# Kernel optimization log

Measured on AMD Instinct MI355X. Metric: run time of the kernel, lower is better.

Reference implementation:

```python
import jax, jax.numpy as jnp
import numpy as np

NL, H, PD, NH, NB = 4, 256, 64, 4, 65
B, L, AA = 2, 384, 48
DH = H // NH
MAX_REL = 32


def _ln(x, g, b):
    m = x.mean(-1, keepdims=True)
    v = ((x - m) ** 2).mean(-1, keepdims=True)
    return (x - m) * jax.lax.rsqrt(v + 1e-5) * g + b


def setup_inputs() -> dict:
    key = jax.random.key(0)
    ks = iter(jax.random.split(key, 64))
    w = lambda *s: jax.random.normal(next(ks), s, jnp.float32) * 0.02
    return dict(
        x=jax.random.normal(next(ks), (B, L, AA), jnp.float32),
        rp_w=w(AA, H), rp_b=jnp.zeros((H,), jnp.float32),
        pos_embed=w(L, H),
        pii_w=w(H, PD), pii_b=jnp.zeros((PD,), jnp.float32),
        pij_w=w(H, PD), pij_b=jnp.zeros((PD,), jnp.float32),
        rel_emb=w(2 * MAX_REL + 2, PD),
        ln_seq_g=jnp.ones((NL, H), jnp.float32), ln_seq_b=jnp.zeros((NL, H), jnp.float32),
        ln_pair_g=jnp.ones((NL, PD), jnp.float32), ln_pair_b=jnp.zeros((NL, PD), jnp.float32),
        pb_w=w(NL, PD, NH),
        in_w=w(NL, H, 3 * H), in_b=jnp.zeros((NL, 3 * H), jnp.float32),
        out_w=w(NL, H, H), out_b=jnp.zeros((NL, H), jnp.float32),
        ff_ln_g=jnp.ones((NL, H), jnp.float32), ff_ln_b=jnp.zeros((NL, H), jnp.float32),
        ff_w1=w(NL, H, 4 * H), ff_b1=jnp.zeros((NL, 4 * H), jnp.float32),
        ff_w2=w(NL, 4 * H, H), ff_b2=jnp.zeros((NL, H), jnp.float32),
        pu_ln_g=jnp.ones((NL, PD), jnp.float32), pu_ln_b=jnp.zeros((NL, PD), jnp.float32),
        pu_w1=w(NL, PD, PD), pu_b1=jnp.zeros((NL, PD), jnp.float32),
        pu_w2=w(NL, PD, PD), pu_b2=jnp.zeros((NL, PD), jnp.float32),
        outer_w=w(NL, 2 * H, PD), outer_b=jnp.zeros((NL, PD), jnp.float32),
        dh_ln_g=jnp.ones((PD,), jnp.float32), dh_ln_b=jnp.zeros((PD,), jnp.float32),
        dh_w1=w(PD, PD), dh_b1=jnp.zeros((PD,), jnp.float32),
        dh_w2=w(PD, NB), dh_b2=jnp.zeros((NB,), jnp.float32),
    )


def reference(x, rp_w, rp_b, pos_embed, pii_w, pii_b, pij_w, pij_b, rel_emb,
              ln_seq_g, ln_seq_b, ln_pair_g, ln_pair_b, pb_w, in_w, in_b,
              out_w, out_b, ff_ln_g, ff_ln_b, ff_w1, ff_b1, ff_w2, ff_b2,
              pu_ln_g, pu_ln_b, pu_w1, pu_b1, pu_w2, pu_b2, outer_w, outer_b,
              dh_ln_g, dh_ln_b, dh_w1, dh_b1, dh_w2, dh_b2):
    Bx, Lx, _ = x.shape
    gelu = lambda t: jax.nn.gelu(t, approximate=False)  # torch nn.GELU default (erf)
    h = x @ rp_w + rp_b + pos_embed[:Lx][None]
    # pair init: outer sum of two linear projections + clipped rel-pos embedding
    pair = (h @ pii_w + pii_b)[:, :, None, :] + (h @ pij_w + pij_b)[:, None, :, :]
    idx = jnp.arange(Lx)
    rel = jnp.clip(idx[None, :] - idx[:, None], -MAX_REL, MAX_REL) + MAX_REL  # (L,L)
    pair = pair + rel_emb[rel][None]
    for i in range(NL):
        seq_n = _ln(h, ln_seq_g[i], ln_seq_b[i])
        bias = _ln(pair, ln_pair_g[i], ln_pair_b[i]) @ pb_w[i]  # (B,L,L,NH)
        mask = bias.mean(axis=(0, 3))  # torch: permute->reshape(B*NH,L,L)->mean(0)
        qkv = seq_n @ in_w[i] + in_b[i]
        q, k, v = jnp.split(qkv, 3, axis=-1)
        q = q.reshape(Bx, Lx, NH, DH)
        k = k.reshape(Bx, Lx, NH, DH)
        v = v.reshape(Bx, Lx, NH, DH)
        scores = jnp.einsum('blhd,bmhd->bhlm', q, k) / float(np.sqrt(DH)) + mask
        attn = jax.nn.softmax(scores, axis=-1)
        o = jnp.einsum('bhlm,bmhd->blhd', attn, v).reshape(Bx, Lx, H)
        h = h + o @ out_w[i] + out_b[i]
        h = h + gelu(_ln(h, ff_ln_g[i], ff_ln_b[i]) @ ff_w1[i] + ff_b1[i]) @ ff_w2[i] + ff_b2[i]
        # outer_proj(cat([h_i, h_j])) == h@W[:H] outer-summed with h@W[H:]
        oi = h @ outer_w[i][:H]
        oj = h @ outer_w[i][H:]
        outer = oi[:, :, None, :] + oj[:, None, :, :] + outer_b[i]  # (B,L,L,PD)
        pair = pair + gelu(_ln(outer, pu_ln_g[i], pu_ln_b[i]) @ pu_w1[i] + pu_b1[i]) @ pu_w2[i] + pu_b2[i]
    logits = gelu(_ln(pair, dh_ln_g, dh_ln_b) @ dh_w1 + dh_b1) @ dh_w2 + dh_b2
    return (logits + jnp.swapaxes(logits, 1, 2)) / 2.0
```

## Files before the change

### kernel.cpp

```cpp
#include <hip/hip_runtime.h>
#include <math.h>

#define LSEQ 384
#define HD 256
#define PDIM 64
#define NHEAD 4
#define NBINS 65
#define BATCH 2
#define NTT (LSEQ / 16)
#define NTRI (NTT * (NTT + 1) / 2)

typedef __attribute__((ext_vector_type(8))) short bf16x8;
typedef __attribute__((ext_vector_type(16))) float f32x16;
typedef __attribute__((ext_vector_type(4))) float f32x4;
typedef __attribute__((ext_vector_type(4))) unsigned u32x4;
typedef __attribute__((ext_vector_type(4))) short s16x4;
#define MFMA32(a, b, c) __builtin_amdgcn_mfma_f32_32x32x16_bf16(a, b, c, 0, 0, 0)

template<int CTRL, int RMASK>
__device__ __forceinline__ float dpp_sum_step(float v) {
    int x = __builtin_amdgcn_update_dpp(0, __float_as_int(v), CTRL, RMASK, 0xf, true);
    return v + __int_as_float(x);
}
template<int CTRL, int RMASK>
__device__ __forceinline__ float dpp_max_step(float v) {
    int x = __builtin_amdgcn_update_dpp(__float_as_int(v), __float_as_int(v), CTRL, RMASK, 0xf, false);
    return fmaxf(v, __int_as_float(x));
}
__device__ __forceinline__ float wsum(float v) {
    v = dpp_sum_step<0x111, 0xf>(v);
    v = dpp_sum_step<0x112, 0xf>(v);
    v = dpp_sum_step<0x114, 0xf>(v);
    v = dpp_sum_step<0x118, 0xf>(v);
    v = dpp_sum_step<0x142, 0xa>(v);
    v = dpp_sum_step<0x143, 0xc>(v);
    return __int_as_float(__builtin_amdgcn_readlane(__float_as_int(v), 63));
}
__device__ __forceinline__ float wmax(float v) {
    v = dpp_max_step<0x111, 0xf>(v);
    v = dpp_max_step<0x112, 0xf>(v);
    v = dpp_max_step<0x114, 0xf>(v);
    v = dpp_max_step<0x118, 0xf>(v);
    v = dpp_max_step<0x142, 0xa>(v);
    v = dpp_max_step<0x143, 0xc>(v);
    return __int_as_float(__builtin_amdgcn_readlane(__float_as_int(v), 63));
}
__device__ __forceinline__ float gelu_erf(float x) {
    return 0.5f * x * (1.0f + erff(x * 0.70710678f));
}

__device__ __forceinline__ unsigned short f2bf(float x) {
    unsigned u = __float_as_uint(x);
    unsigned r = (u + 0x7fff + ((u >> 16) & 1)) >> 16;
    return (unsigned short)r;
}
__device__ __forceinline__ float bf2f(unsigned short h) {
    return __uint_as_float(((unsigned)h) << 16);
}
__device__ __forceinline__ void split_bf(float x, unsigned short& h, unsigned short& l) {
    h = f2bf(x);
    l = f2bf(x - bf2f(h));
}

__device__ __forceinline__ unsigned cvt_pk_bf(float lo, float hi) {
    unsigned r;
    asm("v_cvt_pk_bf16_f32 %0, %1, %2" : "=v"(r) : "v"(lo), "v"(hi));
    return r;
}
__device__ __forceinline__ void pack8(const float* v, u32x4& h, u32x4& l) {
#pragma unroll
    for (int j = 0; j < 4; ++j) {
        float a = v[2 * j], b = v[2 * j + 1];
        unsigned hp = cvt_pk_bf(a, b);
        float ra = a - __uint_as_float(hp << 16);
        float rb = b - __uint_as_float(hp & 0xffff0000u);
        h[j] = hp;
        l[j] = cvt_pk_bf(ra, rb);
    }
}
__device__ __forceinline__ bf16x8 as_bf(u32x4 x) {
    union { u32x4 u; bf16x8 b; } c; c.u = x; return c.b;
}
__device__ __forceinline__ bf16x8 ld8(const short* p) {
    s16x4 a = *(const s16x4*)p;
    s16x4 b = *(const s16x4*)(p + 4);
    bf16x8 r;
    r[0] = a[0]; r[1] = a[1]; r[2] = a[2]; r[3] = a[3];
    r[4] = b[0]; r[5] = b[1]; r[6] = b[2]; r[7] = b[3];
    return r;
}

__global__ void k_h_init(const float* __restrict__ x, const float* __restrict__ rp_w,
                         const float* __restrict__ rp_b, const float* __restrict__ pos,
                         float* __restrict__ h) {
    __shared__ float xs[48];
    int row = blockIdx.x;
    int l = row % LSEQ;
    int t = threadIdx.x;
    if (t < 48) xs[t] = x[row * 48 + t];
    __syncthreads();
    float acc = rp_b[t] + pos[l * HD + t];
#pragma unroll 8
    for (int a = 0; a < 48; ++a) acc += xs[a] * rp_w[a * HD + t];
    h[row * HD + t] = acc;
}

__global__ void k_proj2(const float* __restrict__ h, const float* __restrict__ wA,
                        const float* __restrict__ wB, const float* __restrict__ bA,
                        const float* __restrict__ bB, int center,
                        float* __restrict__ pA, float* __restrict__ pB) {
    __shared__ float hs[HD];
    int row = blockIdx.x;
    int t = threadIdx.x;
    hs[t] = h[row * HD + t];
    hs[t + 128] = h[row * HD + t + 128];
    __syncthreads();
    int col = t & 63;
    const float* w = (t < 64) ? wA : wB;
    const float* bias = (t < 64) ? bA : bB;
    float acc = bias ? bias[col] : 0.0f;
#pragma unroll 8
    for (int a = 0; a < HD; ++a) acc += hs[a] * w[a * PDIM + col];
    if (center) {
        float mean = wsum(acc) * (1.0f / PDIM);
        acc -= mean;
    }
    float* p = (t < 64) ? pA : pB;
    p[row * PDIM + col] = acc;
}

__global__ void __launch_bounds__(64) k_pair_init2(
    const float* __restrict__ pi, const float* __restrict__ pj,
    const float* __restrict__ rel_emb, const float* __restrict__ gpb,
    const float* __restrict__ cbv, float* __restrict__ pair,
    float* __restrict__ mask_out) {
    __shared__ __align__(16) float pt[32][65];
    int blk = blockIdx.x;
    int row = blk / 12, seg = blk % 12;
    int b = row / LSEQ, i = row % LSEQ;
    int t = threadIdx.x;
    int pl = t & 31, hq = t >> 5;
    int j0 = seg * 32;
    float piv = pi[row * 64 + t];
    const float* pjb = pj + ((size_t)b * LSEQ + j0) * 64;
#pragma unroll 8
    for (int j = 0; j < 32; ++j) {
        int r = j0 + j - i; r = r < -32 ? -32 : (r > 32 ? 32 : r); r += 32;
        pt[j][t] = piv + pjb[j * 64 + t] + rel_emb[r * 64 + t];
    }
    __syncthreads();
    float4* dst4 = (float4*)(pair + ((size_t)row * LSEQ + j0) * 64);
    for (int n = t; n < 512; n += 64) {
        int r2 = n >> 4, c4 = (n & 15) << 2;
        float4 g4 = { pt[r2][c4], pt[r2][c4 + 1], pt[r2][c4 + 2], pt[r2][c4 + 3] };
        dst4[n] = g4;
    }
    float vv[32];
    float sv = 0.0f;
#pragma unroll
    for (int c = 0; c < 32; ++c) { vv[c] = pt[pl][hq * 32 + c]; sv += vv[c]; }
    sv += __shfl_xor(sv, 32);
    float mean = sv * (1.0f / PDIM);
    float sd2 = 0.0f, sdg = 0.0f;
#pragma unroll
    for (int c = 0; c < 32; ++c) {
        float d = vv[c] - mean;
        sd2 = fmaf(d, d, sd2);
        sdg = fmaf(d, gpb[hq * 32 + c], sdg);
    }
    sd2 += __shfl_xor(sd2, 32);
    sdg += __shfl_xor(sdg, 32);
    float rsv = rsqrtf(sd2 * (1.0f / PDIM) + 1e-5f);
    float dot = rsv * sdg + cbv[0];
    if (hq == 0)
        atomicAdd(mask_out + i * LSEQ + j0 + pl, dot * (1.0f / (BATCH * NHEAD)));
}

__global__ void k_prep(const float* __restrict__ pu_ln_g, const float* __restrict__ pu_ln_b,
                       const float* __restrict__ pu_w1, const float* __restrict__ pu_b1,
                       const float* __restrict__ pu_w2,
                       const float* __restrict__ dh_ln_g, const float* __restrict__ dh_ln_b,
                       const float* __restrict__ dh_w1, const float* __restrict__ dh_b1,
                       const float* __restrict__ dh_w2,
                       unsigned short* __restrict__ w1hT, unsigned short* __restrict__ w1lT,
                       unsigned short* __restrict__ w2hT, unsigned short* __restrict__ w2lT,
                       float* __restrict__ b1p, float* __restrict__ w2c) {
    int i = blockIdx.x;
    int c = threadIdx.x;
    const float *g, *bb, *w1, *b1, *w2;
    int w2s;
    if (i < 4) { g = pu_ln_g + i * 64; bb = pu_ln_b + i * 64; w1 = pu_w1 + i * 4096;
                 b1 = pu_b1 + i * 64; w2 = pu_w2 + i * 4096; w2s = 64; }
    else       { g = dh_ln_g; bb = dh_ln_b; w1 = dh_w1; b1 = dh_b1; w2 = dh_w2; w2s = 65; }
    float accb = b1[c];
    for (int k = 0; k < 64; ++k) {
        float wv = w1[k * 64 + c];
        accb += bb[k] * wv;
        unsigned short h, l;
        split_bf(g[k] * wv, h, l);
        w1hT[i * 4096 + c * 64 + k] = h;
        w1lT[i * 4096 + c * 64 + k] = l;
        split_bf(w2[k * w2s + c], h, l);
        w2hT[i * 4096 + c * 64 + k] = h;
        w2lT[i * 4096 + c * 64 + k] = l;
    }
    b1p[i * 64 + c] = accb;
    if (i == 4) w2c[c] = dh_w2[c * 65 + 64];
}

__global__ void k_maskprep(const float* __restrict__ g, const float* __restrict__ bb,
                           const float* __restrict__ pbw, float* __restrict__ gp,
                           float* __restrict__ cb) {
    int li = blockIdx.x;
    int c = threadIdx.x;
    const float* pw = pbw + li * PDIM * NHEAD;
    float pbs = pw[c * 4] + pw[c * 4 + 1] + pw[c * 4 + 2] + pw[c * 4 + 3];
    gp[li * 64 + c] = g[li * 64 + c] * pbs;
    float s = wsum(bb[li * 64 + c] * pbs);
    if (c == 0) cb[li] = s;
}

__global__ void k_split_T(const float* __restrict__ src, unsigned short* __restrict__ dh,
                          unsigned short* __restrict__ dl, int K, int N,
                          int tiles_k, int tiles_n, size_t sstride, size_t dstride) {
    __shared__ float lds[64][65];
    int bid = blockIdx.x;
    int tpl = tiles_k * tiles_n;
    int layer = bid / tpl;
    int rest = bid % tpl;
    int kt = rest / tiles_n, nt = rest % tiles_n;
    const float* s = src + layer * sstride;
    int t = threadIdx.x, c = t & 63, r0 = t >> 6;
    for (int r = r0; r < 64; r += 4)
        lds[r][c] = s[(size_t)(kt * 64 + r) * N + nt * 64 + c];
    __syncthreads();
    unsigned short* oh = dh + layer * dstride;
    unsigned short* ol = dl + layer * dstride;
    for (int r = r0; r < 64; r += 4) {
        float v = lds[c][r];
        unsigned short h, l;
        split_bf(v, h, l);
        size_t o = (size_t)(nt * 64 + r) * K + kt * 64 + c;
        oh[o] = h;
        ol[o] = l;
    }
}

template<bool GELU>
__global__ void __launch_bounds__(256) k_gemm(
    const float* __restrict__ X, const unsigned short* __restrict__ wTh,
    const unsigned short* __restrict__ wTl, const float* __restrict__ bias,
    const float* __restrict__ R, float* __restrict__ OUT, int K, int N) {
    int idx = blockIdx.x * 4 + (threadIdx.x >> 6);
    int lane = threadIdx.x & 63;
    int pl = lane & 31, hq = lane >> 5;
    int ntiles = N >> 5;
    int mt = idx / ntiles, nt = idx % ntiles;
    const float* xr = X + (size_t)(mt * 32 + pl) * K + 8 * hq;
    const unsigned short* bh = wTh + (size_t)(nt * 32 + pl) * K + 8 * hq;
    const unsigned short* bl = wTl + (size_t)(nt * 32 + pl) * K + 8 * hq;
    int n = nt * 32 + pl;
    float bv = bias[n];
    f32x16 acc;
#pragma unroll
    for (int r = 0; r < 16; ++r) {
        int mr = mt * 32 + (r & 3) + 8 * (r >> 2) + 4 * hq;
        acc[r] = bv + (R ? R[(size_t)mr * N + n] : 0.0f);
    }
#pragma unroll 4
    for (int s = 0; s < K; s += 16) {
        const f32x4* x4 = (const f32x4*)(xr + s);
        f32x4 xa = x4[0], xb = x4[1];
        float xv[8];
#pragma unroll
        for (int j = 0; j < 4; ++j) { xv[j] = xa[j]; xv[4 + j] = xb[j]; }
        u32x4 ah, al;
        pack8(xv, ah, al);
        bf16x8 bhv = *(const bf16x8*)(bh + s);
        bf16x8 blv = *(const bf16x8*)(bl + s);
        acc = MFMA32(as_bf(ah), bhv, acc);
        acc = MFMA32(as_bf(al), bhv, acc);
        acc = MFMA32(as_bf(ah), blv, acc);
    }
#pragma unroll
    for (int r = 0; r < 16; ++r) {
        int mr = mt * 32 + (r & 3) + 8 * (r >> 2) + 4 * hq;
        float v = acc[r];
        OUT[(size_t)mr * N + n] = GELU ? gelu_erf(v) : v;
    }
}

__global__ void k_ln_seq(const float* __restrict__ h, const float* __restrict__ g,
                         const float* __restrict__ b, float* __restrict__ out) {
    __shared__ float red[8];
    int row = blockIdx.x;
    int t = threadIdx.x;
    int w = t >> 6, lane = t & 63;
    float v = h[row * HD + t];
    float s = wsum(v);
    if (lane == 0) red[w] = s;
    __syncthreads();
    float mean = (red[0] + red[1] + red[2] + red[3]) * (1.0f / HD);
    float d = v - mean;
    float q = wsum(d * d);
    if (lane == 0) red[4 + w] = q;
    __syncthreads();
    float var = (red[4] + red[5] + red[6] + red[7]) * (1.0f / HD);
    out[row * HD + t] = d * rsqrtf(var + 1e-5f) * g[t] + b[t];
}

__global__ void k_attn(const float* __restrict__ qkv, const float* __restrict__ mask,
                       float* __restrict__ o) {
    __shared__ __align__(16) float qs[64];
    __shared__ float sc[LSEQ];
    __shared__ float red[8];
    __shared__ float op[4][64];
    int bid = blockIdx.x;
    int l = bid % LSEQ;
    int nh = (bid / LSEQ) & 3;
    int b = bid / (LSEQ * NHEAD);
    int t = threadIdx.x;
    int w = t >> 6, lane = t & 63;
    const float* qbase = qkv + ((size_t)(b * LSEQ + l)) * 768 + nh * 64;
    if (t < 64) qs[t] = qbase[t];
    __syncthreads();
    float lmax = -1e30f;
    float myv[2];
#pragma unroll
    for (int it = 0; it < 2; ++it) {
        int m = t + it * 256;
        if (m < LSEQ) {
            const float* kb = qkv + ((size_t)(b * LSEQ + m)) * 768 + 256 + nh * 64;
            const float4* k4 = (const float4*)kb;
            const float4* q4 = (const float4*)qs;
            float acc = 0.0f;
#pragma unroll
            for (int a = 0; a < 16; ++a) {
                float4 kv = k4[a], qv = q4[a];
                acc += qv.x * kv.x + qv.y * kv.y + qv.z * kv.z + qv.w * kv.w;
            }
            float s = acc * 0.125f + mask[l * LSEQ + m];
            myv[it] = s;
            lmax = fmaxf(lmax, s);
        } else myv[it] = -1e30f;
    }
    float wm = wmax(lmax);
    if (lane == 0) red[w] = wm;
    __syncthreads();
    float gmax = fmaxf(fmaxf(red[0], red[1]), fmaxf(red[2], red[3]));
    float lsum = 0.0f;
#pragma unroll
    for (int it = 0; it < 2; ++it) {
        int m = t + it * 256;
        if (m < LSEQ) {
            float e = expf(myv[it] - gmax);
            sc[m] = e;
            lsum += e;
        }
    }
    float ws = wsum(lsum);
    if (lane == 0) red[4 + w] = ws;
    __syncthreads();
    float inv = 1.0f / (red[4] + red[5] + red[6] + red[7]);
    int d = t & 63, gq = t >> 6;
    float part = 0.0f;
    for (int m = gq * 96; m < (gq + 1) * 96; ++m)
        part += sc[m] * qkv[((size_t)(b * LSEQ + m)) * 768 + 512 + nh * 64 + d];
    op[gq][d] = part;
    __syncthreads();
    if (t < 64) {
        float ov = (op[0][t] + op[1][t] + op[2][t] + op[3][t]) * inv;
        o[((size_t)(b * LSEQ + l)) * HD + nh * 64 + t] = ov;
    }
}

template<bool DIST>
__global__ void __launch_bounds__(256) k_pair_upd(
    const float* __restrict__ ojc,
    const float* __restrict__ oic,
    const unsigned short* __restrict__ w1hT, const unsigned short* __restrict__ w1lT,
    const float* __restrict__ b1p,
    const unsigned short* __restrict__ w2hT, const unsigned short* __restrict__ w2lT,
    const float* __restrict__ b2, float* __restrict__ pair,
    const float* __restrict__ gpb, const float* __restrict__ cbv,
    float* __restrict__ mask_out,
    const unsigned short* __restrict__ dw1h, const unsigned short* __restrict__ dw1l,
    const float* __restrict__ db1p,
    const unsigned short* __restrict__ dw2h, const unsigned short* __restrict__ dw2l,
    const float* __restrict__ w2c, const float* __restrict__ db2,
    float* __restrict__ outg) {
    __shared__ short lw[4][64][68];
    constexpr int PTR = DIST ? 128 : 1;
    __shared__ __align__(16) float pt[PTR][65];
    int blk = blockIdx.x;
    int row = blk / 3, seg = blk % 3;
    int b = row / LSEQ;
    int t = threadIdx.x;
    int wave = t >> 6, lane = t & 63;
    int pl = lane & 31, hq = lane >> 5;
    int jj = wave * 32 + pl;
    int p = seg * 128 + jj;
    const float* ojr = ojc + ((size_t)b * LSEQ + p) * 64;
    const float* oir = oic + (size_t)row * 64;
    float* prp = pair + ((size_t)row * LSEQ + p) * 64;

    float v[32];
    {
        const f32x4* a4 = (const f32x4*)ojr;
        const f32x4* c4 = (const f32x4*)oir;
#pragma unroll
        for (int s = 0; s < 4; ++s) {
            f32x4 a = a4[4 * s + 2 * hq], aa = a4[4 * s + 2 * hq + 1];
            f32x4 c = c4[4 * s + 2 * hq], cc = c4[4 * s + 2 * hq + 1];
#pragma unroll
            for (int j = 0; j < 4; ++j) {
                v[8 * s + j] = a[j] + c[j];
                v[8 * s + 4 + j] = aa[j] + cc[j];
            }
        }
    }
#define STAGE_W(a2, src) \
    for (int idx = t; idx < 2048; idx += 256) { \
        int rr2 = idx >> 5, cc2 = idx & 31; \
        *(unsigned*)(&lw[a2][rr2][cc2 * 2]) = *(const unsigned*)(src + rr2 * 64 + cc2 * 2); \
    }
    STAGE_W(0, w1hT)
    STAGE_W(1, w1lT)
    STAGE_W(2, w2hT)
    STAGE_W(3, w2lT)

    float ss = 0.0f;
#pragma unroll
    for (int i = 0; i < 32; ++i) ss = fmaf(v[i], v[i], ss);
    ss += __shfl_xor(ss, 32);
    float rs = rsqrtf(ss * (1.0f / PDIM) + 1e-5f);
#pragma unroll
    for (int i = 0; i < 32; ++i) v[i] *= rs;
    u32x4 zh[4], zl[4];
#pragma unroll
    for (int s = 0; s < 4; ++s) pack8(v + 8 * s, zh[s], zl[s]);

    const f32x4* b14 = (const f32x4*)b1p;
    f32x4 bi0[4], bi1[4];
#pragma unroll
    for (int g = 0; g < 4; ++g) { bi0[g] = b14[2 * g + hq]; bi1[g] = b14[8 + 2 * g + hq]; }

    __syncthreads();

    f32x16 acc0, acc1;
#pragma unroll
    for (int r = 0; r < 16; ++r) {
        acc0[r] = bi0[r >> 2][r & 3];
        acc1[r] = bi1[r >> 2][r & 3];
    }
#pragma unroll
    for (int s = 0; s < 4; ++s) {
        int ko = 16 * s + 8 * hq;
        bf16x8 a0h = ld8(&lw[0][pl][ko]);
        bf16x8 a0l = ld8(&lw[1][pl][ko]);
        bf16x8 a1h = ld8(&lw[0][32 + pl][ko]);
        bf16x8 a1l = ld8(&lw[1][32 + pl][ko]);
        bf16x8 zhs = as_bf(zh[s]), zls = as_bf(zl[s]);
        acc0 = MFMA32(a0h, zhs, acc0);
        acc0 = MFMA32(a0h, zls, acc0);
        acc0 = MFMA32(a0l, zhs, acc0);
        acc1 = MFMA32(a1h, zhs, acc1);
        acc1 = MFMA32(a1h, zls, acc1);
        acc1 = MFMA32(a1l, zhs, acc1);
    }
    float u0[16], u1[16];
#pragma unroll
    for (int r = 0; r < 16; ++r) { u0[r] = gelu_erf(acc0[r]); u1[r] = gelu_erf(acc1[r]); }

    f32x4 r0[4], r1[4], q0[4], q1[4];
    {
        const f32x4* pr4 = (const f32x4*)prp;
        const f32x4* b24 = (const f32x4*)b2;
#pragma unroll
        for (int g = 0; g < 4; ++g) {
            r0[g] = pr4[2 * g + hq];
            r1[g] = pr4[8 + 2 * g + hq];
            q0[g] = b24[2 * g + hq];
            q1[g] = b24[8 + 2 * g + hq];
        }
    }

    float rA0[4], rB0[4], rA1[4], rB1[4];
#pragma unroll
    for (int i = 0; i < 4; ++i) {
        rA0[i] = __shfl_xor(hq ? u0[i] : u0[4 + i], 32);
        rB0[i] = __shfl_xor(hq ? u0[8 + i] : u0[12 + i], 32);
        rA1[i] = __shfl_xor(hq ? u1[i] : u1[4 + i], 32);
        rB1[i] = __shfl_xor(hq ? u1[8 + i] : u1[12 + i], 32);
    }
    u32x4 uh[4], ul[4];
#pragma unroll
    for (int s = 0; s < 4; ++s) {
        int tt = s >> 1, q = s & 1;
        float fg[8];
#pragma unroll
        for (int i = 0; i < 4; ++i) {
            float own_f = q ? (tt ? u1[8 + i] : u0[8 + i]) : (tt ? u1[i] : u0[i]);
            float own_s = q ? (tt ? u1[12 + i] : u0[12 + i]) : (tt ? u1[4 + i] : u0[4 + i]);
            float rcv   = q ? (tt ? rB1[i] : rB0[i]) : (tt ? rA1[i] : rA0[i]);
            fg[i]     = hq ? rcv : own_f;
            fg[4 + i] = hq ? own_s : rcv;
        }
        pack8(fg, uh[s], ul[s]);
    }

    f32x16 c0, c1;
#pragma unroll
    for (int r = 0; r < 16; ++r) {
        int g = r >> 2, i = r & 3;
        c0[r] = q0[g][i] + r0[g][i];
        c1[r] = q1[g][i] + r1[g][i];
    }
#pragma unroll
    for (int s = 0; s < 4; ++s) {
        int ko = 16 * s + 8 * hq;
        bf16x8 a0h = ld8(&lw[2][pl][ko]);
        bf16x8 a0l = ld8(&lw[3][pl][ko]);
        bf16x8 a1h = ld8(&lw[2][32 + pl][ko]);
        bf16x8 a1l = ld8(&lw[3][32 + pl][ko]);
        bf16x8 uhs = as_bf(uh[s]), uls = as_bf(ul[s]);
        c0 = MFMA32(a0h, uhs, c0);
        c0 = MFMA32(a0h, uls, c0);
        c0 = MFMA32(a0l, uhs, c0);
        c1 = MFMA32(a1h, uhs, c1);
        c1 = MFMA32(a1h, uls, c1);
        c1 = MFMA32(a1l, uhs, c1);
    }

    if constexpr (!DIST) {
        const f32x4* gp4 = (const f32x4*)gpb;
        f32x4 gp0[4], gp1[4];
#pragma unroll
        for (int g = 0; g < 4; ++g) { gp0[g] = gp4[2 * g + hq]; gp1[g] = gp4[8 + 2 * g + hq]; }
        float sv = 0.0f;
#pragma unroll
        for (int r = 0; r < 16; ++r) sv += c0[r] + c1[r];
        sv += __shfl_xor(sv, 32);
        float mean = sv * (1.0f / PDIM);
        float sd2 = 0.0f, sdg = 0.0f;
#pragma unroll 4
        for (int r = 0; r < 16; ++r) {
            int g = r >> 2, i = r & 3;
            float d0 = c0[r] - mean, d1 = c1[r] - mean;
            sd2 = fmaf(d0, d0, sd2);
            sd2 = fmaf(d1, d1, sd2);
            sdg = fmaf(d0, gp0[g][i], sdg);
            sdg = fmaf(d1, gp1[g][i], sdg);
        }
        sd2 += __shfl_xor(sd2, 32);
        sdg += __shfl_xor(sdg, 32);
        float rsv = rsqrtf(sd2 * (1.0f / PDIM) + 1e-5f);
        float dot = rsv * sdg + cbv[0];
        if (hq == 0)
            atomicAdd(mask_out + (row % LSEQ) * LSEQ + p, dot * (1.0f / (BATCH * NHEAD)));
        f32x4* pw4 = (f32x4*)prp;
#pragma unroll
        for (int g = 0; g < 4; ++g) {
            f32x4 s0, s1;
#pragma unroll
            for (int i = 0; i < 4; ++i) { s0[i] = c0[4 * g + i]; s1[i] = c1[4 * g + i]; }
            pw4[2 * g + hq] = s0;
            pw4[8 + 2 * g + hq] = s1;
        }
    } else {
#pragma unroll
        for (int r = 0; r < 16; ++r) {
            int rr = (r & 3) + 8 * (r >> 2) + 4 * hq;
            pt[jj][rr] = c0[r];
            pt[jj][32 + rr] = c1[r];
        }
        float v2[32];
#pragma unroll
        for (int s = 0; s < 4; ++s) {
            int k0 = 16 * s + 8 * hq;
#pragma unroll
            for (int j = 0; j < 8; ++j) v2[8 * s + j] = pt[jj][k0 + j];
        }
        float sm = 0.0f;
#pragma unroll
        for (int i = 0; i < 32; ++i) sm += v2[i];
        sm += __shfl_xor(sm, 32);
        float mean = sm * (1.0f / PDIM);
        float ss2 = 0.0f;
#pragma unroll
        for (int i = 0; i < 32; ++i) { v2[i] -= mean; ss2 = fmaf(v2[i], v2[i], ss2); }
        ss2 += __shfl_xor(ss2, 32);
        float rs2 = rsqrtf(ss2 * (1.0f / PDIM) + 1e-5f);
#pragma unroll
        for (int i = 0; i < 32; ++i) v2[i] *= rs2;
#pragma unroll
        for (int s = 0; s < 4; ++s) pack8(v2 + 8 * s, zh[s], zl[s]);

        __syncthreads();
        STAGE_W(0, dw1h)
        STAGE_W(1, dw1l)
        STAGE_W(2, dw2h)
        STAGE_W(3, dw2l)
        const f32x4* d14 = (const f32x4*)db1p;
        const f32x4* d24 = (const f32x4*)db2;
        const f32x4* wc4 = (const f32x4*)w2c;
        f32x4 di0[4], di1[4], e0[4], e1[4], wc0[4], wc1[4];
#pragma unroll
        for (int g = 0; g < 4; ++g) {
            di0[g] = d14[2 * g + hq]; di1[g] = d14[8 + 2 * g + hq];
            e0[g] = d24[2 * g + hq];  e1[g] = d24[8 + 2 * g + hq];
            wc0[g] = wc4[2 * g + hq]; wc1[g] = wc4[8 + 2 * g + hq];
        }
        __syncthreads();

#pragma unroll
        for (int r = 0; r < 16; ++r) {
            acc0[r] = di0[r >> 2][r & 3];
            acc1[r] = di1[r >> 2][r & 3];
        }
#pragma unroll
        for (int s = 0; s < 4; ++s) {
            int ko = 16 * s + 8 * hq;
            bf16x8 a0h = ld8(&lw[0][pl][ko]);
            bf16x8 a0l = ld8(&lw[1][pl][ko]);
            bf16x8 a1h = ld8(&lw[0][32 + pl][ko]);
            bf16x8 a1l = ld8(&lw[1][32 + pl][ko]);
            bf16x8 zhs = as_bf(zh[s]), zls = as_bf(zl[s]);
            acc0 = MFMA32(a0h, zhs, acc0);
            acc0 = MFMA32(a0h, zls, acc0);
            acc0 = MFMA32(a0l, zhs, acc0);
            acc1 = MFMA32(a1h, zhs, acc1);
            acc1 = MFMA32(a1h, zls, acc1);
            acc1 = MFMA32(a1l, zhs, acc1);
        }
        float p64 = 0.0f;
#pragma unroll
        for (int r = 0; r < 16; ++r) {
            int g = r >> 2, i = r & 3;
            u0[r] = gelu_erf(acc0[r]);
            u1[r] = gelu_erf(acc1[r]);
            p64 = fmaf(u0[r], wc0[g][i], p64);
            p64 = fmaf(u1[r], wc1[g][i], p64);
        }
        p64 += __shfl_xor(p64, 32);
#pragma unroll
        for (int i = 0; i < 4; ++i) {
            rA0[i] = __shfl_xor(hq ? u0[i] : u0[4 + i], 32);
            rB0[i] = __shfl_xor(hq ? u0[8 + i] : u0[12 + i], 32);
            rA1[i] = __shfl_xor(hq ? u1[i] : u1[4 + i], 32);
            rB1[i] = __shfl_xor(hq ? u1[8 + i] : u1[12 + i], 32);
        }
#pragma unroll
        for (int s = 0; s < 4; ++s) {
            int tt = s >> 1, q = s & 1;
            float fg[8];
#pragma unroll
            for (int i = 0; i < 4; ++i) {
                float own_f = q ? (tt ? u1[8 + i] : u0[8 + i]) : (tt ? u1[i] : u0[i]);
                float own_s = q ? (tt ? u1[12 + i] : u0[12 + i]) : (tt ? u1[4 + i] : u0[4 + i]);
                float rcv   = q ? (tt ? rB1[i] : rB0[i]) : (tt ? rA1[i] : rA0[i]);
                fg[i]     = hq ? rcv : own_f;
                fg[4 + i] = hq ? own_s : rcv;
            }
            pack8(fg, uh[s], ul[s]);
        }
#pragma unroll
        for (int r = 0; r < 16; ++r) {
            c0[r] = e0[r >> 2][r & 3];
            c1[r] = e1[r >> 2][r & 3];
        }
#pragma unroll
        for (int s = 0; s < 4; ++s) {
            int ko = 16 * s + 8 * hq;
            bf16x8 a0h = ld8(&lw[2][pl][ko]);
            bf16x8 a0l = ld8(&lw[3][pl][ko]);
            bf16x8 a1h = ld8(&lw[2][32 + pl][ko]);
            bf16x8 a1l = ld8(&lw[3][32 + pl][ko]);
            bf16x8 uhs = as_bf(uh[s]), uls = as_bf(ul[s]);
            c0 = MFMA32(a0h, uhs, c0);
            c0 = MFMA32(a0h, uls, c0);
            c0 = MFMA32(a0l, uhs, c0);
            c1 = MFMA32(a1h, uhs, c1);
            c1 = MFMA32(a1h, uls, c1);
            c1 = MFMA32(a1l, uhs, c1);
        }
#pragma unroll
        for (int r = 0; r < 16; ++r) {
            int rr = (r & 3) + 8 * (r >> 2) + 4 * hq;
            pt[jj][rr] = c0[r];
            pt[jj][32 + rr] = c1[r];
        }
        if (hq == 0) pt[jj][64] = p64 + db2[64];
        __syncthreads();
        float4* dst = (float4*)(outg + ((size_t)row * LSEQ + seg * 128) * NBINS);
        const float4* srcl = (const float4*)&pt[0][0];
        for (int n = t; n < 128 * NBINS / 4; n += 256) dst[n] = srcl[n];
    }
#undef STAGE_W
}

__global__ void k_sym(float* __restrict__ out) {
    int u = blockIdx.x;
    int b = 0;
    if (u >= NTRI) { b = 1; u -= NTRI; }
    int lt = 0, rem = NTT;
    while (u >= rem) { u -= rem; ++lt; --rem; }
    int mt = lt + u;
    int t = threadIdx.x;
    int g = t >> 6, lane = t & 63;
    float* ob = out + (size_t)b * LSEQ * LSEQ * NBINS;
    for (int e = g; e < 256; e += 4) {
        int i = e >> 4, j = e & 15;
        if (lt == mt && j < i) continue;
        size_t ia = ((size_t)(lt * 16 + i) * LSEQ + (mt * 16 + j)) * NBINS;
        size_t ib = ((size_t)(mt * 16 + j) * LSEQ + (lt * 16 + i)) * NBINS;
        for (int k = lane; k < NBINS; k += 64) {
            float a = ob[ia + k], c = ob[ib + k];
            float vv = 0.5f * (a + c);
            ob[ia + k] = vv;
            if (ia != ib) ob[ib + k] = vv;
        }
    }
}

extern "C" void kernel_launch(void* const* d_in, const int* in_sizes, int n_in,
                              void* d_out, int out_size, void* d_ws, size_t ws_size,
                              hipStream_t stream) {
    const float* x        = (const float*)d_in[0];
    const float* rp_w     = (const float*)d_in[1];
    const float* rp_b     = (const float*)d_in[2];
    const float* pos      = (const float*)d_in[3];
    const float* pii_w    = (const float*)d_in[4];
    const float* pii_b    = (const float*)d_in[5];
    const float* pij_w    = (const float*)d_in[6];
    const float* pij_b    = (const float*)d_in[7];
    const float* rel_emb  = (const float*)d_in[8];
    const float* ln_seq_g = (const float*)d_in[9];
    const float* ln_seq_b = (const float*)d_in[10];
    const float* ln_pair_g= (const float*)d_in[11];
    const float* ln_pair_b= (const float*)d_in[12];
    const float* pb_w     = (const float*)d_in[13];
    const float* in_w     = (const float*)d_in[14];
    const float* in_b     = (const float*)d_in[15];
    const float* out_w    = (const float*)d_in[16];
    const float* out_b    = (const float*)d_in[17];
    const float* ff_ln_g  = (const float*)d_in[18];
    const float* ff_ln_b  = (const float*)d_in[19];
    const float* ff_w1    = (const float*)d_in[20];
    const float* ff_b1    = (const float*)d_in[21];
    const float* ff_w2    = (const float*)d_in[22];
    const float* ff_b2    = (const float*)d_in[23];
    const float* pu_ln_g  = (const float*)d_in[24];
    const float* pu_ln_b  = (const float*)d_in[25];
    const float* pu_w1    = (const float*)d_in[26];
    const float* pu_b1    = (const float*)d_in[27];
    const float* pu_w2    = (const float*)d_in[28];
    const float* pu_b2    = (const float*)d_in[29];
    const float* outer_w  = (const float*)d_in[30];
    const float* outer_b  = (const float*)d_in[31];
    const float* dh_ln_g  = (const float*)d_in[32];
    const float* dh_ln_b  = (const float*)d_in[33];
    const float* dh_w1    = (const float*)d_in[34];
    const float* dh_b1    = (const float*)d_in[35];
    const float* dh_w2    = (const float*)d_in[36];
    const float* dh_b2    = (const float*)d_in[37];
    float* outp = (float*)d_out;

    float* W = (float*)d_ws;
    float* h    = W;  W += BATCH * LSEQ * HD;
    float* sn   = W;  W += BATCH * LSEQ * HD;
    float* qkv  = W;  W += BATCH * LSEQ * 3 * HD;
    float* ob   = W;  W += BATCH * LSEQ * HD;
    float* mid  = W;  W += BATCH * LSEQ * 4 * HD;
    float* maskA= W;  W += LSEQ * LSEQ;
    float* maskB= W;  W += LSEQ * LSEQ;
    float* poi  = W;  W += BATCH * LSEQ * PDIM;
    float* poj  = W;  W += BATCH * LSEQ * PDIM;
    float* b1p  = W;  W += 5 * 64;
    float* w2c  = W;  W += 64;
    float* gpb  = W;  W += 4 * 64;
    float* cbv  = W;  W += 64;
    unsigned short* w1hT = (unsigned short*)W;  W += 5 * 2048;
    unsigned short* w1lT = (unsigned short*)W;  W += 5 * 2048;
    unsigned short* w2hT = (unsigned short*)W;  W += 5 * 2048;
    unsigned short* w2lT = (unsigned short*)W;  W += 5 * 2048;
    unsigned short* qwT_h = (unsigned short*)W;  W += 4 * 196608 / 2;
    unsigned short* qwT_l = (unsigned short*)W;  W += 4 * 196608 / 2;
    unsigned short* owT_h = (unsigned short*)W;  W += 4 * 65536 / 2;
    unsigned short* owT_l = (unsigned short*)W;  W += 4 * 65536 / 2;
    unsigned short* f1T_h = (unsigned short*)W;  W += 4 * 262144 / 2;
    unsigned short* f1T_l = (unsigned short*)W;  W += 4 * 262144 / 2;
    unsigned short* f2T_h = (unsigned short*)W;  W += 4 * 262144 / 2;
    unsigned short* f2T_l = (unsigned short*)W;  W += 4 * 262144 / 2;
    float* pair = W;  W += (size_t)BATCH * LSEQ * LSEQ * PDIM;

    const int rows = BATCH * LSEQ;

    k_prep<<<5, 64, 0, stream>>>(pu_ln_g, pu_ln_b, pu_w1, pu_b1, pu_w2,
                                 dh_ln_g, dh_ln_b, dh_w1, dh_b1, dh_w2,
                                 w1hT, w1lT, w2hT, w2lT, b1p, w2c);
    k_maskprep<<<4, 64, 0, stream>>>(ln_pair_g, ln_pair_b, pb_w, gpb, cbv);
    k_split_T<<<4 * 4 * 12, 256, 0, stream>>>(in_w,  qwT_h, qwT_l, 256, 768,  4, 12, 196608, 196608);
    k_split_T<<<4 * 4 * 4,  256, 0, stream>>>(out_w, owT_h, owT_l, 256, 256,  4, 4,  65536,  65536);
    k_split_T<<<4 * 4 * 16, 256, 0, stream>>>(ff_w1, f1T_h, f1T_l, 256, 1024, 4, 16, 262144, 262144);
    k_split_T<<<4 * 16 * 4, 256, 0, stream>>>(ff_w2, f2T_h, f2T_l, 1024, 256, 16, 4, 262144, 262144);
    k_h_init<<<rows, 256, 0, stream>>>(x, rp_w, rp_b, pos, h);
    k_proj2<<<rows, 128, 0, stream>>>(h, pii_w, pij_w, pii_b, pij_b, 0, poi, poj);
    hipMemsetAsync(maskA, 0, LSEQ * LSEQ * sizeof(float), stream);
    k_pair_init2<<<rows * 12, 64, 0, stream>>>(poi, poj, rel_emb, gpb, cbv, pair, maskA);

    float* mcur = maskA;
    float* mnext = maskB;
    for (int i = 0; i < 4; ++i) {
        k_ln_seq<<<rows, 256, 0, stream>>>(h, ln_seq_g + i * HD, ln_seq_b + i * HD, sn);
        k_gemm<false><<<144, 256, 0, stream>>>(sn, qwT_h + i * 196608, qwT_l + i * 196608,
                                               in_b + i * 768, nullptr, qkv, 256, 768);
        k_attn<<<BATCH * NHEAD * LSEQ, 256, 0, stream>>>(qkv, mcur, ob);
        k_gemm<false><<<48, 256, 0, stream>>>(ob, owT_h + i * 65536, owT_l + i * 65536,
                                              out_b + i * 256, h, h, 256, 256);
        k_ln_seq<<<rows, 256, 0, stream>>>(h, ff_ln_g + i * HD, ff_ln_b + i * HD, sn);
        k_gemm<true><<<192, 256, 0, stream>>>(sn, f1T_h + i * 262144, f1T_l + i * 262144,
                                              ff_b1 + i * 1024, nullptr, mid, 256, 1024);
        k_gemm<false><<<48, 256, 0, stream>>>(mid, f2T_h + i * 262144, f2T_l + i * 262144,
                                              ff_b2 + i * 256, h, h, 1024, 256);
        k_proj2<<<rows, 128, 0, stream>>>(h, outer_w + i * 2 * HD * PDIM,
                                          outer_w + i * 2 * HD * PDIM + HD * PDIM,
                                          outer_b + i * PDIM, nullptr, 1, poi, poj);
        if (i < 3) {
            hipMemsetAsync(mnext, 0, LSEQ * LSEQ * sizeof(float), stream);
            k_pair_upd<false><<<rows * 3, 256, 0, stream>>>(
                poj, poi,
                w1hT + i * 4096, w1lT + i * 4096, b1p + i * 64,
                w2hT + i * 4096, w2lT + i * 4096, pu_b2 + i * PDIM, pair,
                gpb + (i + 1) * 64, cbv + (i + 1), mnext,
                nullptr, nullptr, nullptr, nullptr, nullptr, nullptr, nullptr, nullptr);
            float* tmp = mcur; mcur = mnext; mnext = tmp;
        } else {
            k_pair_upd<true><<<rows * 3, 256, 0, stream>>>(
                poj, poi,
                w1hT + 3 * 4096, w1lT + 3 * 4096, b1p + 3 * 64,
                w2hT + 3 * 4096, w2lT + 3 * 4096, pu_b2 + 3 * PDIM, pair,
                nullptr, nullptr, nullptr,
                w1hT + 4 * 4096, w1lT + 4 * 4096, b1p + 4 * 64,
                w2hT + 4 * 4096, w2lT + 4 * 4096, w2c, dh_b2, outp);
        }
    }

    k_sym<<<2 * NTRI, 256, 0, stream>>>(outp);
}
```

Baseline: 1.117 ms.

## Halve pair-update LDS footprint, use shuffles for transpose, single-wave GEMM blocks

The pair-update kernel now stages only two weight matrices (hi/lo) in shared memory at a time, reloading the second layer's weights after a barrier. This halves static LDS usage so more blocks can be resident per CU. The distogram path replaces an LDS round-trip transpose with cross-half-wave shuffles, and the output tile aliases the same buffer. The GEMM kernel changes from four waves per block to one wave per block, with four times as many blocks. The cost is extra barriers and serialized weight staging in the pair kernel.

```diff
diff --git a/kernel.cpp b/kernel.cpp
--- a/kernel.cpp
+++ b/kernel.cpp
@@ -247,11 +247,11 @@
 }
 
 template<bool GELU>
-__global__ void __launch_bounds__(256) k_gemm(
+__global__ void __launch_bounds__(64) k_gemm(
     const float* __restrict__ X, const unsigned short* __restrict__ wTh,
     const unsigned short* __restrict__ wTl, const float* __restrict__ bias,
     const float* __restrict__ R, float* __restrict__ OUT, int K, int N) {
-    int idx = blockIdx.x * 4 + (threadIdx.x >> 6);
+    int idx = blockIdx.x;
     int lane = threadIdx.x & 63;
     int pl = lane & 31, hq = lane >> 5;
     int ntiles = N >> 5;
@@ -389,9 +389,8 @@
     const unsigned short* __restrict__ dw2h, const unsigned short* __restrict__ dw2l,
     const float* __restrict__ w2c, const float* __restrict__ db2,
     float* __restrict__ outg) {
-    __shared__ short lw[4][64][68];
-    constexpr int PTR = DIST ? 128 : 1;
-    __shared__ __align__(16) float pt[PTR][65];
+    __shared__ __align__(16) char smem[DIST ? 33344 : 17472];
+    short (*lw)[64][68] = (short (*)[64][68])smem;
     int blk = blockIdx.x;
     int row = blk / 3, seg = blk % 3;
     int b = row / LSEQ;
@@ -404,6 +403,13 @@
     const float* oir = oic + (size_t)row * 64;
     float* prp = pair + ((size_t)row * LSEQ + p) * 64;
 
+#define STAGE2(srcA, srcB) \
+    for (int idx = t; idx < 2048; idx += 256) { \
+        int rr2 = idx >> 5, cc2 = (idx & 31) * 2; \
+        *(unsigned*)&lw[0][rr2][cc2] = *(const unsigned*)(srcA + rr2 * 64 + cc2); \
+        *(unsigned*)&lw[1][rr2][cc2] = *(const unsigned*)(srcB + rr2 * 64 + cc2); \
+    }
+
     float v[32];
     {
         const f32x4* a4 = (const f32x4*)ojr;
@@ -419,15 +425,7 @@
             }
         }
     }
-#define STAGE_W(a2, src) \
-    for (int idx = t; idx < 2048; idx += 256) { \
-        int rr2 = idx >> 5, cc2 = idx & 31; \
-        *(unsigned*)(&lw[a2][rr2][cc2 * 2]) = *(const unsigned*)(src + rr2 * 64 + cc2 * 2); \
-    }
-    STAGE_W(0, w1hT)
-    STAGE_W(1, w1lT)
-    STAGE_W(2, w2hT)
-    STAGE_W(3, w2lT)
+    STAGE2(w1hT, w1lT)
 
     float ss = 0.0f;
 #pragma unroll
@@ -468,6 +466,9 @@
         acc1 = MFMA32(a1h, zls, acc1);
         acc1 = MFMA32(a1l, zhs, acc1);
     }
+    __syncthreads();
+    STAGE2(w2hT, w2lT)
+
     float u0[16], u1[16];
 #pragma unroll
     for (int r = 0; r < 16; ++r) { u0[r] = gelu_erf(acc0[r]); u1[r] = gelu_erf(acc1[r]); }
@@ -509,6 +510,8 @@
         pack8(fg, uh[s], ul[s]);
     }
 
+    __syncthreads();
+
     f32x16 c0, c1;
 #pragma unroll
     for (int r = 0; r < 16; ++r) {
@@ -519,10 +522,10 @@
 #pragma unroll
     for (int s = 0; s < 4; ++s) {
         int ko = 16 * s + 8 * hq;
-        bf16x8 a0h = ld8(&lw[2][pl][ko]);
-        bf16x8 a0l = ld8(&lw[3][pl][ko]);
-        bf16x8 a1h = ld8(&lw[2][32 + pl][ko]);
-        bf16x8 a1l = ld8(&lw[3][32 + pl][ko]);
+        bf16x8 a0h = ld8(&lw[0][pl][ko]);
+        bf16x8 a0l = ld8(&lw[1][pl][ko]);
+        bf16x8 a1h = ld8(&lw[0][32 + pl][ko]);
+        bf16x8 a1l = ld8(&lw[1][32 + pl][ko]);
         bf16x8 uhs = as_bf(uh[s]), uls = as_bf(ul[s]);
         c0 = MFMA32(a0h, uhs, c0);
         c0 = MFMA32(a0h, uls, c0);
@@ -568,19 +571,29 @@
             pw4[8 + 2 * g + hq] = s1;
         }
     } else {
-#pragma unroll
-        for (int r = 0; r < 16; ++r) {
-            int rr = (r & 3) + 8 * (r >> 2) + 4 * hq;
-            pt[jj][rr] = c0[r];
-            pt[jj][32 + rr] = c1[r];
+        float ra[4], rb[4], rc[4], rd[4];
+#pragma unroll
+        for (int i = 0; i < 4; ++i) {
+            ra[i] = __shfl_xor(hq ? c0[i] : c0[4 + i], 32);
+            rb[i] = __shfl_xor(hq ? c0[8 + i] : c0[12 + i], 32);
+            rc[i] = __shfl_xor(hq ? c1[i] : c1[4 + i], 32);
+            rd[i] = __shfl_xor(hq ? c1[8 + i] : c1[12 + i], 32);
         }
         float v2[32];
 #pragma unroll
-        for (int s = 0; s < 4; ++s) {
-            int k0 = 16 * s + 8 * hq;
-#pragma unroll
-            for (int j = 0; j < 8; ++j) v2[8 * s + j] = pt[jj][k0 + j];
-        }
+        for (int i = 0; i < 4; ++i) {
+            v2[i]      = hq ? ra[i] : c0[i];
+            v2[4 + i]  = hq ? c0[4 + i] : ra[i];
+            v2[8 + i]  = hq ? rb[i] : c0[8 + i];
+            v2[12 + i] = hq ? c0[12 + i] : rb[i];
+            v2[16 + i] = hq ? rc[i] : c1[i];
+            v2[20 + i] = hq ? c1[4 + i] : rc[i];
+            v2[24 + i] = hq ? rd[i] : c1[8 + i];
+            v2[28 + i] = hq ? c1[12 + i] : rd[i];
+        }
+        __syncthreads();
+        STAGE2(dw1h, dw1l)
+
         float sm = 0.0f;
 #pragma unroll
         for (int i = 0; i < 32; ++i) sm += v2[i];
@@ -596,11 +609,6 @@
 #pragma unroll
         for (int s = 0; s < 4; ++s) pack8(v2 + 8 * s, zh[s], zl[s]);
 
-        __syncthreads();
-        STAGE_W(0, dw1h)
-        STAGE_W(1, dw1l)
-        STAGE_W(2, dw2h)
-        STAGE_W(3, dw2l)
         const f32x4* d14 = (const f32x4*)db1p;
         const f32x4* d24 = (const f32x4*)db2;
         const f32x4* wc4 = (const f32x4*)w2c;
@@ -633,6 +641,9 @@
             acc1 = MFMA32(a1h, zls, acc1);
             acc1 = MFMA32(a1l, zhs, acc1);
         }
+        __syncthreads();
+        STAGE2(dw2h, dw2l)
+
         float p64 = 0.0f;
 #pragma unroll
         for (int r = 0; r < 16; ++r) {
@@ -664,6 +675,8 @@
             }
             pack8(fg, uh[s], ul[s]);
         }
+        __syncthreads();
+
 #pragma unroll
         for (int r = 0; r < 16; ++r) {
             c0[r] = e0[r >> 2][r & 3];
@@ -672,10 +685,10 @@
 #pragma unroll
         for (int s = 0; s < 4; ++s) {
             int ko = 16 * s + 8 * hq;
-            bf16x8 a0h = ld8(&lw[2][pl][ko]);
-            bf16x8 a0l = ld8(&lw[3][pl][ko]);
-            bf16x8 a1h = ld8(&lw[2][32 + pl][ko]);
-            bf16x8 a1l = ld8(&lw[3][32 + pl][ko]);
+            bf16x8 a0h = ld8(&lw[0][pl][ko]);
+            bf16x8 a0l = ld8(&lw[1][pl][ko]);
+            bf16x8 a1h = ld8(&lw[0][32 + pl][ko]);
+            bf16x8 a1l = ld8(&lw[1][32 + pl][ko]);
             bf16x8 uhs = as_bf(uh[s]), uls = as_bf(ul[s]);
             c0 = MFMA32(a0h, uhs, c0);
             c0 = MFMA32(a0h, uls, c0);
@@ -684,6 +697,8 @@
             c1 = MFMA32(a1h, uls, c1);
             c1 = MFMA32(a1l, uhs, c1);
         }
+        __syncthreads();
+        float (*pt)[65] = (float (*)[65])smem;
 #pragma unroll
         for (int r = 0; r < 16; ++r) {
             int rr = (r & 3) + 8 * (r >> 2) + 4 * hq;
@@ -696,7 +711,7 @@
         const float4* srcl = (const float4*)&pt[0][0];
         for (int n = t; n < 128 * NBINS / 4; n += 256) dst[n] = srcl[n];
     }
-#undef STAGE_W
+#undef STAGE2
 }
 
 __global__ void k_sym(float* __restrict__ out) {
@@ -813,15 +828,15 @@
     float* mnext = maskB;
     for (int i = 0; i < 4; ++i) {
         k_ln_seq<<<rows, 256, 0, stream>>>(h, ln_seq_g + i * HD, ln_seq_b + i * HD, sn);
-        k_gemm<false><<<144, 256, 0, stream>>>(sn, qwT_h + i * 196608, qwT_l + i * 196608,
-                                               in_b + i * 768, nullptr, qkv, 256, 768);
+        k_gemm<false><<<576, 64, 0, stream>>>(sn, qwT_h + i * 196608, qwT_l + i * 196608,
+                                              in_b + i * 768, nullptr, qkv, 256, 768);
         k_attn<<<BATCH * NHEAD * LSEQ, 256, 0, stream>>>(qkv, mcur, ob);
-        k_gemm<false><<<48, 256, 0, stream>>>(ob, owT_h + i * 65536, owT_l + i * 65536,
+        k_gemm<false><<<192, 64, 0, stream>>>(ob, owT_h + i * 65536, owT_l + i * 65536,
                                               out_b + i * 256, h, h, 256, 256);
         k_ln_seq<<<rows, 256, 0, stream>>>(h, ff_ln_g + i * HD, ff_ln_b + i * HD, sn);
-        k_gemm<true><<<192, 256, 0, stream>>>(sn, f1T_h + i * 262144, f1T_l + i * 262144,
-                                              ff_b1 + i * 1024, nullptr, mid, 256, 1024);
-        k_gemm<false><<<48, 256, 0, stream>>>(mid, f2T_h + i * 262144, f2T_l + i * 262144,
+        k_gemm<true><<<768, 64, 0, stream>>>(sn, f1T_h + i * 262144, f1T_l + i * 262144,
+                                             ff_b1 + i * 1024, nullptr, mid, 256, 1024);
+        k_gemm<false><<<192, 64, 0, stream>>>(mid, f2T_h + i * 262144, f2T_l + i * 262144,
                                               ff_b2 + i * 256, h, h, 1024, 256);
         k_proj2<<<rows, 128, 0, stream>>>(h, outer_w + i * 2 * HD * PDIM,
                                           outer_w + i * 2 * HD * PDIM + HD * PDIM,
```

Result: faster. 1.050 ms (-5.9%).
